# Kernel optimization log

Measured on AMD Instinct MI355X. Metric: run time of the kernel, lower is better.

The kernel has to match this reference:

```python
import jax, jax.numpy as jnp
import numpy as np
from jax import lax

B = 1024          # batch size (queries / docs)
H = 1536          # GRU hidden = embedding dim (hard-coded in module)
MAX_NEGS = 32     # max negatives per query
TEMP = 0.05       # opt.temperature


def setup_inputs() -> dict:
    key = jax.random.key(0)
    ks = jax.random.split(key, 8)
    rng = np.random.default_rng(0)
    lens = rng.integers(0, MAX_NEGS + 1, size=B)  # variable-length negs, some zero
    total = int(lens.sum())
    s = 0.02
    return {
        "q_emb": jax.random.normal(ks[0], (B, H), jnp.float32),
        "k_emb": jax.random.normal(ks[1], (B, H), jnp.float32),
        "inpn_emb": jax.random.normal(ks[2], (total, H), jnp.float32),
        "len_input_negs": jnp.asarray(lens, jnp.int32),
        "W_ih": jax.random.normal(ks[3], (3 * H, H), jnp.float32) * s,
        "W_hh": jax.random.normal(ks[4], (3 * H, H), jnp.float32) * s,
        "b_ih": jax.random.normal(ks[5], (3 * H,), jnp.float32) * s,
        "b_hh": jax.random.normal(ks[6], (3 * H,), jnp.float32) * s,
    }


def _ragged_gru_final(inpn_emb, lens, h0, W_ih, W_hh, b_ih, b_hh):
    """Batched equivalent of the per-sample torch GRU loop.

    For sample i: run a 1-layer GRU over inpn_emb[start_i:start_i+len_i]
    with initial hidden h0[i]; return final hidden (h0[i] if len_i == 0).
    """
    total = inpn_emb.shape[0]
    offsets = jnp.concatenate([jnp.zeros((1,), jnp.int32),
                               jnp.cumsum(lens)[:-1].astype(jnp.int32)])
    t = jnp.arange(MAX_NEGS, dtype=jnp.int32)
    idx = jnp.clip(offsets[:, None] + t[None, :], 0, total - 1)   # [B, Lmax]
    mask = t[None, :] < lens[:, None]                              # [B, Lmax]
    x_pad = inpn_emb[idx]                                          # [B, Lmax, H]

    def step(h, xm):
        x, m = xm                                  # x: [B,H], m: [B]
        gi = x @ W_ih.T + b_ih                     # [B, 3H]
        gh = h @ W_hh.T + b_hh                     # [B, 3H]
        i_r, i_z, i_n = jnp.split(gi, 3, axis=-1)
        h_r, h_z, h_n = jnp.split(gh, 3, axis=-1)
        r = jax.nn.sigmoid(i_r + h_r)
        z = jax.nn.sigmoid(i_z + h_z)
        n = jnp.tanh(i_n + r * h_n)
        h_new = (1.0 - z) * n + z * h
        h = jnp.where(m[:, None], h_new, h)        # freeze past end of seq
        return h, None

    h_final, _ = lax.scan(step, h0,
                          (x_pad.transpose(1, 0, 2), mask.T))
    return h_final


def reference(q_emb, k_emb, inpn_emb, len_input_negs, W_ih, W_hh, b_ih, b_hh):
    qemb = _ragged_gru_final(inpn_emb, len_input_negs, q_emb,
                             W_ih, W_hh, b_ih, b_hh)          # [B, H]
    scores = jnp.einsum("id,jd->ij", qemb / TEMP, k_emb)       # [B, B]
    labels = jnp.arange(B)
    logp = jax.nn.log_softmax(scores, axis=-1)
    loss = -jnp.mean(jnp.take_along_axis(logp, labels[:, None], axis=1))
    return loss
```

## Files before the change

### kernel.cpp

```cpp
#include <hip/hip_runtime.h>
#include <hip/hip_bf16.h>

#define B_SZ 1024
#define H_DIM 1536
#define H3 (3*H_DIM)
#define LMAX 32
#define TEMP_INV 20.0f

typedef __attribute__((ext_vector_type(4))) float f32x4;
typedef __attribute__((ext_vector_type(8))) short short8;
typedef unsigned short u16;
typedef unsigned int u32;

__device__ __forceinline__ u16 f2bf(float f){
  union { float f; u32 u; } v; v.f = f;
  u32 r = (v.u + 0x7FFFu + ((v.u >> 16) & 1u)) >> 16;
  return (u16)r;
}
__device__ __forceinline__ u32 pack2(float lo, float hi){
  return (u32)f2bf(lo) | ((u32)f2bf(hi) << 16);
}
__device__ __forceinline__ float bf2f(u16 b){
  union { u32 u; float f; } v; v.u = ((u32)b) << 16; return v.f;
}
__device__ __forceinline__ float sigm(float x){ return 1.f / (1.f + __expf(-x)); }

__device__ __forceinline__ void gload_lds16(const void* g, void* l){
  __builtin_amdgcn_global_load_lds(
      (const __attribute__((address_space(1))) void*)g,
      (__attribute__((address_space(3))) void*)l, 16, 0, 0);
}

__global__ void sort_kernel(const int* __restrict__ lens, int* __restrict__ rank,
                            int* __restrict__ cnt_arr, int* __restrict__ tstart,
                            int* __restrict__ rowmap)
{
  __shared__ int wavecnt[33][17];
  __shared__ int bintot[33];
  __shared__ int scnt[LMAX];
  __shared__ int sts[LMAX];
  __shared__ int soff[B_SZ];
  int i = threadIdx.x;
  int li = lens[i];
  int w = i >> 6, lane = i & 63;

  if (i < 33 * 17) ((int*)wavecnt)[i] = 0;
  __syncthreads();

  int mypre = 0;
  #pragma unroll 1
  for (int b = 0; b <= 32; ++b) {
    unsigned long long m = __ballot(li == b);
    if (lane == 0) wavecnt[b][w] = __popcll(m);
    if (b == li) mypre = __popcll(m & ((1ull << lane) - 1ull));
  }
  __syncthreads();

  if (i < 33) {
    int c = 0;
    #pragma unroll 1
    for (int w2 = 0; w2 < 16; ++w2) c += wavecnt[i][w2];
    bintot[i] = c;
  }
  __syncthreads();

  int wpre = 0;
  #pragma unroll 1
  for (int w2 = 0; w2 < w; ++w2) wpre += wavecnt[li][w2];
  int base = 0;
  #pragma unroll 1
  for (int b = li + 1; b <= 32; ++b) base += bintot[b];
  int r = base + wpre + mypre;
  rank[i] = r;

  if (i < LMAX) {
    int c = 0;
    #pragma unroll 1
    for (int b = i + 1; b <= 32; ++b) c += bintot[b];
    scnt[i] = c; cnt_arr[i] = c;
  }
  __syncthreads();
  if (i == 0) {
    int acc = 0;
    for (int t = 0; t < LMAX; ++t) { sts[t] = acc; tstart[t] = acc; acc += scnt[t]; }
  }

  soff[i] = li;
  __syncthreads();
  for (int off = 1; off < B_SZ; off <<= 1) {
    int v = (i >= off) ? soff[i - off] : 0;
    __syncthreads();
    soff[i] += v;
    __syncthreads();
  }
  int myoff = soff[i] - li;
  for (int t = 0; t < li; ++t)
    rowmap[myoff + t] = sts[t] + r;
}

__global__ void prep_kernel(const float* __restrict__ wih, const float* __restrict__ whh,
                            const float* __restrict__ kemb, const float* __restrict__ qemb,
                            const int* __restrict__ rank,
                            u16* __restrict__ wih_bf, u16* __restrict__ whh_bf,
                            u16* __restrict__ k_bf, u16* __restrict__ h0)
{
  size_t o = ((size_t)blockIdx.x * 256 + threadIdx.x) * 8;
  if (o < (size_t)H3 * H_DIM) {
    float4 a0 = *(const float4*)(wih + o), a1 = *(const float4*)(wih + o + 4);
    *(uint4*)(wih_bf + o) = make_uint4(pack2(a0.x,a0.y), pack2(a0.z,a0.w),
                                       pack2(a1.x,a1.y), pack2(a1.z,a1.w));
    float4 b0 = *(const float4*)(whh + o), b1 = *(const float4*)(whh + o + 4);
    *(uint4*)(whh_bf + o) = make_uint4(pack2(b0.x,b0.y), pack2(b0.z,b0.w),
                                       pack2(b1.x,b1.y), pack2(b1.z,b1.w));
  }
  if (o < (size_t)B_SZ * H_DIM) {
    float4 k0 = *(const float4*)(kemb + o), k1 = *(const float4*)(kemb + o + 4);
    *(uint4*)(k_bf + o) = make_uint4(pack2(k0.x,k0.y), pack2(k0.z,k0.w),
                                     pack2(k1.x,k1.y), pack2(k1.z,k1.w));
    int i = (int)(o / H_DIM), col = (int)(o % H_DIM);
    float4 q0 = *(const float4*)(qemb + o), q1 = *(const float4*)(qemb + o + 4);
    *(uint4*)(h0 + (size_t)rank[i] * H_DIM + col) =
        make_uint4(pack2(q0.x,q0.y), pack2(q0.z,q0.w),
                   pack2(q1.x,q1.y), pack2(q1.z,q1.w));
  }
}

__global__ void convx_kernel(const float* __restrict__ x, const int* __restrict__ rowmap,
                             u16* __restrict__ xt, int total){
  size_t o = ((size_t)blockIdx.x * 256 + threadIdx.x) * 8;
  int row = (int)(o / H_DIM), col = (int)(o % H_DIM);
  if (row < total) {
    float4 a0 = *(const float4*)(x + o), a1 = *(const float4*)(x + o + 4);
    *(uint4*)(xt + (size_t)rowmap[row] * H_DIM + col) =
        make_uint4(pack2(a0.x,a0.y), pack2(a0.z,a0.w),
                   pack2(a1.x,a1.y), pack2(a1.z,a1.w));
  } else {
    *(uint4*)(xt + o) = make_uint4(0,0,0,0);
  }
}

__global__ __launch_bounds__(256, 2) void gi_gemm_kernel(
    const u16* __restrict__ x_bf, const u16* __restrict__ wih_bf,
    const float* __restrict__ b_ih, u16* __restrict__ gi, int nblk_m)
{
  int nblk = nblk_m * 36;
  int id = blockIdx.x;
  int q8 = nblk >> 3, r8 = nblk & 7;
  int xcd = id & 7, off = id >> 3;
  int swz = (xcd < r8) ? (xcd * (q8 + 1) + off) : (r8 * (q8 + 1) + (xcd - r8) * q8 + off);
  int bx = swz / 36, by = swz % 36;

  __shared__ u16 lds[2 * 128 * 64];
  char* ldsb = (char*)lds;
  int tid = threadIdx.x, wid = tid >> 6, lane = tid & 63;
  int wm = wid >> 1, wn = wid & 1;
  int lrow = lane & 15, lkh = lane >> 4;
  f32x4 acc[4][4] = {};

  for (int kt = 0; kt < 24; ++kt) {
    int k0 = kt * 64;
    #pragma unroll
    for (int it = 0; it < 8; ++it) {
      int cb = it * 256 + wid * 64;
      int c  = cb + lane;
      int isB = c >> 10;
      int cc  = c & 1023;
      int row = cc >> 3, slot = cc & 7;
      const u16* src = isB ? (wih_bf + (size_t)(by * 128 + row) * H_DIM)
                           : (x_bf  + (size_t)(bx * 128 + row) * H_DIM);
      src += k0 + ((slot ^ (row & 7)) << 3);
      gload_lds16(src, ldsb + (size_t)cb * 16);
    }
    __syncthreads();
    #pragma unroll
    for (int qq = 0; qq < 2; ++qq) {
      short8 a[4], b[4];
      int slot = qq * 4 + lkh;
      #pragma unroll
      for (int m = 0; m < 4; ++m) {
        int row = wm * 64 + m * 16 + lrow;
        a[m] = *(const short8*)(ldsb + row * 128 + ((slot ^ (row & 7)) << 4));
      }
      #pragma unroll
      for (int n = 0; n < 4; ++n) {
        int row = wn * 64 + n * 16 + lrow;
        b[n] = *(const short8*)(ldsb + 16384 + row * 128 + ((slot ^ (row & 7)) << 4));
      }
      #pragma unroll
      for (int m = 0; m < 4; ++m)
        #pragma unroll
        for (int n = 0; n < 4; ++n)
          acc[m][n] = __builtin_amdgcn_mfma_f32_16x16x32_bf16(a[m], b[n], acc[m][n], 0,0,0);
    }
    __syncthreads();
  }
  #pragma unroll
  for (int n = 0; n < 4; ++n) {
    int j = by * 128 + wn * 64 + n * 16 + lrow;
    float bias = b_ih[j];
    #pragma unroll
    for (int m = 0; m < 4; ++m)
      #pragma unroll
      for (int r4 = 0; r4 < 4; ++r4) {
        int rowg = bx * 128 + wm * 64 + m * 16 + lkh * 4 + r4;
        gi[(size_t)rowg * 4608 + j] = f2bf(acc[m][n][r4] + bias);
      }
  }
}

__global__ __launch_bounds__(256, 4) void gh_step_kernel(
    const u16* __restrict__ h_cur, u16* __restrict__ h_nxt,
    const u16* __restrict__ whh_bf, const u16* __restrict__ gi,
    const float* __restrict__ b_hh,
    const int* __restrict__ cnt_arr, const int* __restrict__ tstart, int t)
{
  int cnt = cnt_arr[t];
  int bid = blockIdx.x;
  int x8 = bid & 7, jj = bid >> 3;
  int ct = x8 * 6 + jj % 6;
  int bx = jj / 6;
  if (bx * 64 >= cnt) return;
  int ts = tstart[t];

  __shared__ u16 lds[2 * 10240];
  char* ldsb = (char*)lds;

  int tid = threadIdx.x, wid = tid >> 6, lane = tid & 63;
  int wm = wid >> 1, wn = wid & 1;
  int lrow = lane & 15, lkh = lane >> 4;
  f32x4 acc[3][2] = {};
  float hold[2][4];

  auto STAGE = [&](int buf, int kt){
    int k0 = kt * 64;
    char* base = ldsb + buf * 20480;
    #pragma unroll
    for (int it = 0; it < 5; ++it) {
      int cb = it * 256 + wid * 64;
      int c  = cb + lane;
      const u16* src;
      if (c < 512) {
        int row = c >> 3, slot = c & 7;
        int ridx = bx * 64 + row; if (ridx >= cnt) ridx = cnt - 1;
        src = h_cur + (size_t)ridx * H_DIM + k0 + ((slot ^ (row & 7)) << 3);
      } else {
        int w = c - 512;
        int slab = w >> 8, row = (w >> 3) & 31, slot = w & 7;
        src = whh_bf + (size_t)(slab * H_DIM + ct * 32 + row) * H_DIM
              + k0 + ((slot ^ (row & 7)) << 3);
      }
      gload_lds16(src, base + (size_t)cb * 16);
    }
  };

  auto COMPUTE = [&](int buf){
    char* base = ldsb + buf * 20480;
    #pragma unroll
    for (int qq = 0; qq < 2; ++qq) {
      short8 ah[2], bw[3];
      int slot = qq * 4 + lkh;
      #pragma unroll
      for (int m = 0; m < 2; ++m) {
        int row = wm * 32 + m * 16 + lrow;
        ah[m] = *(const short8*)(base + row * 128 + ((slot ^ (row & 7)) << 4));
      }
      {
        int row = wn * 16 + lrow;
        int byte = row * 128 + ((slot ^ (row & 7)) << 4);
        #pragma unroll
        for (int s = 0; s < 3; ++s)
          bw[s] = *(const short8*)(base + 8192 + s * 4096 + byte);
      }
      #pragma unroll
      for (int s = 0; s < 3; ++s)
        #pragma unroll
        for (int m = 0; m < 2; ++m)
          acc[s][m] = __builtin_amdgcn_mfma_f32_16x16x32_bf16(
              ah[m], bw[s], acc[s][m], 0, 0, 0);
    }
  };

  STAGE(0, 0);
  for (int kt = 0; kt < 24; ++kt) {
    if (kt + 1 < 24) {
      STAGE((kt + 1) & 1, kt + 1);
      asm volatile("s_waitcnt vmcnt(5)" ::: "memory");
    } else {
      asm volatile("s_waitcnt vmcnt(0)" ::: "memory");
    }
    __builtin_amdgcn_sched_barrier(0);
    __builtin_amdgcn_s_barrier();
    __builtin_amdgcn_sched_barrier(0);
    COMPUTE(kt & 1);
    if (kt == (ct >> 1)) {
      char* base = ldsb + (kt & 1) * 20480;
      int col = ((ct & 1) << 5) + wn * 16 + lrow;
      int slot = col >> 3, within = col & 7;
      #pragma unroll
      for (int m = 0; m < 2; ++m)
        #pragma unroll
        for (int r4 = 0; r4 < 4; ++r4) {
          int row = wm * 32 + m * 16 + lkh * 4 + r4;
          hold[m][r4] = bf2f(*(const u16*)(base + row * 128 +
                             ((slot ^ (row & 7)) << 4) + within * 2));
        }
    }
    __builtin_amdgcn_s_barrier();
    __builtin_amdgcn_sched_barrier(0);
  }

  {
    int lc = wn * 16 + lrow;
    int j = ct * 32 + lc;
    float bhr = b_hh[j], bhz = b_hh[H_DIM + j], bhn = b_hh[2*H_DIM + j];
    #pragma unroll
    for (int m = 0; m < 2; ++m)
      #pragma unroll
      for (int r4 = 0; r4 < 4; ++r4) {
        int lm = wm * 32 + m * 16 + lkh * 4 + r4;
        int ridx = bx * 64 + lm;
        if (ridx < cnt) {
          size_t gr = (size_t)(ts + ridx) * 4608;
          float gir = bf2f(__builtin_nontemporal_load(&gi[gr + j]));
          float giz = bf2f(__builtin_nontemporal_load(&gi[gr + H_DIM + j]));
          float gin = bf2f(__builtin_nontemporal_load(&gi[gr + 2*H_DIM + j]));
          float rr = sigm(gir + acc[0][m][r4] + bhr);
          float zz = sigm(giz + acc[1][m][r4] + bhz);
          float nn = tanhf(gin + rr * (acc[2][m][r4] + bhn));
          h_nxt[(size_t)ridx * H_DIM + j] = f2bf((1.f - zz) * nn + zz * hold[m][r4]);
        }
      }
  }
}

__global__ __launch_bounds__(256, 2) void scores_kernel(
    const u16* __restrict__ h0, const u16* __restrict__ h1,
    const int* __restrict__ lens, const int* __restrict__ rank,
    const u16* __restrict__ k_bf, float* __restrict__ scores)
{
  int bx = blockIdx.x, by = blockIdx.y;
  __shared__ u16 lds[2 * 64 * 64];
  char* ldsb = (char*)lds;
  int tid = threadIdx.x, wid = tid >> 6, lane = tid & 63;
  int wm = wid >> 1, wn = wid & 1;
  int lrow = lane & 15, lkh = lane >> 4;
  f32x4 acc[2][2] = {};

  for (int kt = 0; kt < 24; ++kt) {
    int k0 = kt * 64;
    #pragma unroll
    for (int it = 0; it < 4; ++it) {
      int cb = it * 256 + wid * 64;
      int c  = cb + lane;
      int isB = c >> 9;
      int cc  = c & 511;
      int row = cc >> 3, slot = cc & 7;
      const u16* src;
      if (!isB) {
        int g = bx * 64 + row;
        src = ((lens[g] & 1) ? h1 : h0) + (size_t)rank[g] * H_DIM;
      } else {
        src = k_bf + (size_t)(by * 64 + row) * H_DIM;
      }
      src += k0 + ((slot ^ (row & 7)) << 3);
      gload_lds16(src, ldsb + (size_t)cb * 16);
    }
    __syncthreads();
    #pragma unroll
    for (int qq = 0; qq < 2; ++qq) {
      short8 a[2], b[2];
      int slot = qq * 4 + lkh;
      #pragma unroll
      for (int m = 0; m < 2; ++m) {
        int row = wm * 32 + m * 16 + lrow;
        a[m] = *(const short8*)(ldsb + row * 128 + ((slot ^ (row & 7)) << 4));
      }
      #pragma unroll
      for (int n = 0; n < 2; ++n) {
        int row = wn * 32 + n * 16 + lrow;
        b[n] = *(const short8*)(ldsb + 8192 + row * 128 + ((slot ^ (row & 7)) << 4));
      }
      #pragma unroll
      for (int m = 0; m < 2; ++m)
        #pragma unroll
        for (int n = 0; n < 2; ++n)
          acc[m][n] = __builtin_amdgcn_mfma_f32_16x16x32_bf16(a[m], b[n], acc[m][n], 0,0,0);
    }
    __syncthreads();
  }
  #pragma unroll
  for (int m = 0; m < 2; ++m)
    #pragma unroll
    for (int n = 0; n < 2; ++n) {
      int col = by * 64 + wn * 32 + n * 16 + lrow;
      #pragma unroll
      for (int r4 = 0; r4 < 4; ++r4) {
        int rowg = bx * 64 + wm * 32 + m * 16 + lkh * 4 + r4;
        scores[(size_t)rowg * B_SZ + col] = acc[m][n][r4] * TEMP_INV;
      }
    }
}

__global__ void softmax_kernel(const float* __restrict__ scores, float* __restrict__ row_loss){
  int i = blockIdx.x;
  int tid = threadIdx.x;
  const float* row = scores + (size_t)i * B_SZ;
  __shared__ float red[4];
  float m = -INFINITY;
  for (int j = tid; j < B_SZ; j += 256) m = fmaxf(m, row[j]);
  for (int off = 32; off; off >>= 1) m = fmaxf(m, __shfl_xor(m, off));
  if ((tid & 63) == 0) red[tid >> 6] = m;
  __syncthreads();
  m = fmaxf(fmaxf(red[0], red[1]), fmaxf(red[2], red[3]));
  __syncthreads();
  float s = 0.f;
  for (int j = tid; j < B_SZ; j += 256) s += __expf(row[j] - m);
  for (int off = 32; off; off >>= 1) s += __shfl_xor(s, off);
  if ((tid & 63) == 0) red[tid >> 6] = s;
  __syncthreads();
  if (tid == 0) {
    float S = red[0] + red[1] + red[2] + red[3];
    row_loss[i] = m + __logf(S) - row[i];
  }
}

__global__ void final_kernel(const float* __restrict__ row_loss, float* __restrict__ out){
  __shared__ float s[B_SZ];
  int i = threadIdx.x;
  s[i] = row_loss[i]; __syncthreads();
  for (int off = 512; off; off >>= 1) {
    if (i < off) s[i] += s[i + off];
    __syncthreads();
  }
  if (i == 0) out[0] = s[0] * (1.0f / B_SZ);
}

extern "C" void kernel_launch(void* const* d_in, const int* in_sizes, int n_in,
                              void* d_out, int out_size, void* d_ws, size_t ws_size,
                              hipStream_t stream) {
  const float* q_emb = (const float*)d_in[0];
  const float* k_emb = (const float*)d_in[1];
  const float* inpn  = (const float*)d_in[2];
  const int*   lens  = (const int*)d_in[3];
  const float* wih   = (const float*)d_in[4];
  const float* whh   = (const float*)d_in[5];
  const float* bih   = (const float*)d_in[6];
  const float* bhh   = (const float*)d_in[7];
  float* out = (float*)d_out;

  int total  = in_sizes[2] / H_DIM;
  int mtiles = (total + 127) / 128;
  int Mpad   = mtiles * 128;

  char* p = (char*)d_ws;
  auto alloc = [&](size_t bytes){ char* r = p; p += (bytes + 255) & ~(size_t)255; return r; };
  int* rank      = (int*)alloc(B_SZ * 4);
  int* cnt_arr   = (int*)alloc(LMAX * 4);
  int* tstart    = (int*)alloc(LMAX * 4);
  int* rowmap    = (int*)alloc((size_t)Mpad * 4);
  u16* hbuf0     = (u16*)alloc((size_t)B_SZ * H_DIM * 2);
  u16* hbuf1     = (u16*)alloc((size_t)B_SZ * H_DIM * 2);
  u16* wih_bf    = (u16*)alloc((size_t)H3 * H_DIM * 2);
  u16* whh_bf    = (u16*)alloc((size_t)H3 * H_DIM * 2);
  u16* k_bf      = (u16*)alloc((size_t)B_SZ * H_DIM * 2);
  u16* xt        = (u16*)alloc((size_t)Mpad * H_DIM * 2);
  u16* gi        = (u16*)alloc((size_t)Mpad * H3 * 2);
  float* scores  = (float*)alloc((size_t)B_SZ * B_SZ * 4);
  float* row_loss= (float*)alloc(B_SZ * 4);
  if ((size_t)(p - (char*)d_ws) > ws_size) return;

  sort_kernel<<<1, B_SZ, 0, stream>>>(lens, rank, cnt_arr, tstart, rowmap);
  prep_kernel<<<(H3 * H_DIM / 8) / 256, 256, 0, stream>>>(
      wih, whh, k_emb, q_emb, rank, wih_bf, whh_bf, k_bf, hbuf0);
  convx_kernel<<<((size_t)Mpad * H_DIM / 8) / 256, 256, 0, stream>>>(
      inpn, rowmap, xt, total);

  gi_gemm_kernel<<<mtiles * 36, 256, 0, stream>>>(xt, wih_bf, bih, gi, mtiles);

  for (int t = 0; t < LMAX; ++t) {
    u16* hc = (t & 1) ? hbuf1 : hbuf0;
    u16* hn = (t & 1) ? hbuf0 : hbuf1;
    gh_step_kernel<<<768, 256, 0, stream>>>(
        hc, hn, whh_bf, gi, bhh, cnt_arr, tstart, t);
  }

  scores_kernel<<<dim3(B_SZ / 64, B_SZ / 64), 256, 0, stream>>>(
      hbuf0, hbuf1, lens, rank, k_bf, scores);
  softmax_kernel<<<B_SZ, 256, 0, stream>>>(scores, row_loss);
  final_kernel<<<1, B_SZ, 0, stream>>>(row_loss, out);
}
```

Baseline: 1.044 ms.

## Prefetch gi in GRU step, double-buffer scores GEMM, fuse final reduction

Three separate changes. The GRU step kernel now loads its gi gate inputs before the K loop, so their latency is hidden behind the W_hh GEMM instead of sitting in the epilogue. The scores GEMM gets double-buffered LDS with async staging and explicit waitcnt/barriers. The final reduction kernel is removed in favour of per-row atomicAdd into a memset output. Together these add register pressure, nondeterministic float summation order and an extra memset.

```diff
diff --git a/kernel.cpp b/kernel.cpp
--- a/kernel.cpp
+++ b/kernel.cpp
@@ -281,6 +281,25 @@
   };
 
   STAGE(0, 0);
+
+  int lc = wn * 16 + lrow;
+  int j = ct * 32 + lc;
+  u16 pgir[2][4], pgiz[2][4], pgin[2][4];
+  asm volatile("" ::: "memory");
+  float bhr = b_hh[j], bhz = b_hh[H_DIM + j], bhn = b_hh[2*H_DIM + j];
+  #pragma unroll
+  for (int m = 0; m < 2; ++m)
+    #pragma unroll
+    for (int r4 = 0; r4 < 4; ++r4) {
+      int lm = wm * 32 + m * 16 + lkh * 4 + r4;
+      int ridx = bx * 64 + lm; if (ridx >= cnt) ridx = cnt - 1;
+      size_t gr = (size_t)(ts + ridx) * 4608;
+      pgir[m][r4] = __builtin_nontemporal_load(&gi[gr + j]);
+      pgiz[m][r4] = __builtin_nontemporal_load(&gi[gr + H_DIM + j]);
+      pgin[m][r4] = __builtin_nontemporal_load(&gi[gr + 2*H_DIM + j]);
+    }
+  asm volatile("" ::: "memory");
+
   for (int kt = 0; kt < 24; ++kt) {
     if (kt + 1 < 24) {
       STAGE((kt + 1) & 1, kt + 1);
@@ -309,28 +328,19 @@
     __builtin_amdgcn_sched_barrier(0);
   }
 
-  {
-    int lc = wn * 16 + lrow;
-    int j = ct * 32 + lc;
-    float bhr = b_hh[j], bhz = b_hh[H_DIM + j], bhn = b_hh[2*H_DIM + j];
-    #pragma unroll
-    for (int m = 0; m < 2; ++m)
-      #pragma unroll
-      for (int r4 = 0; r4 < 4; ++r4) {
-        int lm = wm * 32 + m * 16 + lkh * 4 + r4;
-        int ridx = bx * 64 + lm;
-        if (ridx < cnt) {
-          size_t gr = (size_t)(ts + ridx) * 4608;
-          float gir = bf2f(__builtin_nontemporal_load(&gi[gr + j]));
-          float giz = bf2f(__builtin_nontemporal_load(&gi[gr + H_DIM + j]));
-          float gin = bf2f(__builtin_nontemporal_load(&gi[gr + 2*H_DIM + j]));
-          float rr = sigm(gir + acc[0][m][r4] + bhr);
-          float zz = sigm(giz + acc[1][m][r4] + bhz);
-          float nn = tanhf(gin + rr * (acc[2][m][r4] + bhn));
-          h_nxt[(size_t)ridx * H_DIM + j] = f2bf((1.f - zz) * nn + zz * hold[m][r4]);
-        }
-      }
-  }
+  #pragma unroll
+  for (int m = 0; m < 2; ++m)
+    #pragma unroll
+    for (int r4 = 0; r4 < 4; ++r4) {
+      int lm = wm * 32 + m * 16 + lkh * 4 + r4;
+      int ridx = bx * 64 + lm;
+      if (ridx < cnt) {
+        float rr = sigm(bf2f(pgir[m][r4]) + acc[0][m][r4] + bhr);
+        float zz = sigm(bf2f(pgiz[m][r4]) + acc[1][m][r4] + bhz);
+        float nn = tanhf(bf2f(pgin[m][r4]) + rr * (acc[2][m][r4] + bhn));
+        h_nxt[(size_t)ridx * H_DIM + j] = f2bf((1.f - zz) * nn + zz * hold[m][r4]);
+      }
+    }
 }
 
 __global__ __launch_bounds__(256, 2) void scores_kernel(
@@ -339,15 +349,16 @@
     const u16* __restrict__ k_bf, float* __restrict__ scores)
 {
   int bx = blockIdx.x, by = blockIdx.y;
-  __shared__ u16 lds[2 * 64 * 64];
+  __shared__ u16 lds[2 * 2 * 64 * 64];
   char* ldsb = (char*)lds;
   int tid = threadIdx.x, wid = tid >> 6, lane = tid & 63;
   int wm = wid >> 1, wn = wid & 1;
   int lrow = lane & 15, lkh = lane >> 4;
   f32x4 acc[2][2] = {};
 
-  for (int kt = 0; kt < 24; ++kt) {
+  auto STAGE = [&](int buf, int kt){
     int k0 = kt * 64;
+    char* base = ldsb + buf * 16384;
     #pragma unroll
     for (int it = 0; it < 4; ++it) {
       int cb = it * 256 + wid * 64;
@@ -363,9 +374,12 @@
         src = k_bf + (size_t)(by * 64 + row) * H_DIM;
       }
       src += k0 + ((slot ^ (row & 7)) << 3);
-      gload_lds16(src, ldsb + (size_t)cb * 16);
-    }
-    __syncthreads();
+      gload_lds16(src, base + (size_t)cb * 16);
+    }
+  };
+
+  auto COMPUTE = [&](int buf){
+    char* base = ldsb + buf * 16384;
     #pragma unroll
     for (int qq = 0; qq < 2; ++qq) {
       short8 a[2], b[2];
@@ -373,12 +387,12 @@
       #pragma unroll
       for (int m = 0; m < 2; ++m) {
         int row = wm * 32 + m * 16 + lrow;
-        a[m] = *(const short8*)(ldsb + row * 128 + ((slot ^ (row & 7)) << 4));
+        a[m] = *(const short8*)(base + row * 128 + ((slot ^ (row & 7)) << 4));
       }
       #pragma unroll
       for (int n = 0; n < 2; ++n) {
         int row = wn * 32 + n * 16 + lrow;
-        b[n] = *(const short8*)(ldsb + 8192 + row * 128 + ((slot ^ (row & 7)) << 4));
+        b[n] = *(const short8*)(base + 8192 + row * 128 + ((slot ^ (row & 7)) << 4));
       }
       #pragma unroll
       for (int m = 0; m < 2; ++m)
@@ -386,7 +400,22 @@
         for (int n = 0; n < 2; ++n)
           acc[m][n] = __builtin_amdgcn_mfma_f32_16x16x32_bf16(a[m], b[n], acc[m][n], 0,0,0);
     }
-    __syncthreads();
+  };
+
+  STAGE(0, 0);
+  for (int kt = 0; kt < 24; ++kt) {
+    if (kt + 1 < 24) {
+      STAGE((kt + 1) & 1, kt + 1);
+      asm volatile("s_waitcnt vmcnt(4)" ::: "memory");
+    } else {
+      asm volatile("s_waitcnt vmcnt(0)" ::: "memory");
+    }
+    __builtin_amdgcn_sched_barrier(0);
+    __builtin_amdgcn_s_barrier();
+    __builtin_amdgcn_sched_barrier(0);
+    COMPUTE(kt & 1);
+    __builtin_amdgcn_s_barrier();
+    __builtin_amdgcn_sched_barrier(0);
   }
   #pragma unroll
   for (int m = 0; m < 2; ++m)
@@ -401,7 +430,7 @@
     }
 }
 
-__global__ void softmax_kernel(const float* __restrict__ scores, float* __restrict__ row_loss){
+__global__ void softmax_kernel(const float* __restrict__ scores, float* __restrict__ out){
   int i = blockIdx.x;
   int tid = threadIdx.x;
   const float* row = scores + (size_t)i * B_SZ;
@@ -420,19 +449,8 @@
   __syncthreads();
   if (tid == 0) {
     float S = red[0] + red[1] + red[2] + red[3];
-    row_loss[i] = m + __logf(S) - row[i];
-  }
-}
-
-__global__ void final_kernel(const float* __restrict__ row_loss, float* __restrict__ out){
-  __shared__ float s[B_SZ];
-  int i = threadIdx.x;
-  s[i] = row_loss[i]; __syncthreads();
-  for (int off = 512; off; off >>= 1) {
-    if (i < off) s[i] += s[i + off];
-    __syncthreads();
-  }
-  if (i == 0) out[0] = s[0] * (1.0f / B_SZ);
+    atomicAdd(out, (m + __logf(S) - row[i]) * (1.0f / B_SZ));
+  }
 }
 
 extern "C" void kernel_launch(void* const* d_in, const int* in_sizes, int n_in,
@@ -466,8 +484,9 @@
   u16* xt        = (u16*)alloc((size_t)Mpad * H_DIM * 2);
   u16* gi        = (u16*)alloc((size_t)Mpad * H3 * 2);
   float* scores  = (float*)alloc((size_t)B_SZ * B_SZ * 4);
-  float* row_loss= (float*)alloc(B_SZ * 4);
   if ((size_t)(p - (char*)d_ws) > ws_size) return;
+
+  hipMemsetAsync(out, 0, 4, stream);
 
   sort_kernel<<<1, B_SZ, 0, stream>>>(lens, rank, cnt_arr, tstart, rowmap);
   prep_kernel<<<(H3 * H_DIM / 8) / 256, 256, 0, stream>>>(
@@ -486,6 +505,5 @@
 
   scores_kernel<<<dim3(B_SZ / 64, B_SZ / 64), 256, 0, stream>>>(
       hbuf0, hbuf1, lens, rank, k_bf, scores);
-  softmax_kernel<<<B_SZ, 256, 0, stream>>>(scores, row_loss);
-  final_kernel<<<1, B_SZ, 0, stream>>>(row_loss, out);
-}
+  softmax_kernel<<<B_SZ, 256, 0, stream>>>(scores, out);
+}
```

Result: faster. 965.3 us (-7.5%).
